# Performance work log

Hardware: AMD Instinct MI355X
Metric: run time of the kernel (lower is better)

## Reference

```python
import jax, jax.numpy as jnp
import numpy as np
import math

B, I, C = 64, 512, 32
PRED, PL, ST, NH = 96, 16, 8, 8
WKS = (24, 168, 336)
PN = (I + ST - PL) // ST + 1  # 64 patches (padding_patch='end')

def _gelu(x):
    return jax.nn.gelu(x, approximate=False)  # torch nn.GELU default (erf)

def _ln(x, g, b, eps=1e-5):
    m = x.mean(-1, keepdims=True)
    v = ((x - m) ** 2).mean(-1, keepdims=True)
    return (x - m) / jnp.sqrt(v + eps) * g + b

def setup_inputs() -> dict:
    keys = jax.random.split(jax.random.key(0), 64)
    ki = iter(keys)
    def nrm(sh, sc=0.02):
        return (jax.random.normal(next(ki), sh) * sc).astype(jnp.float32)
    inp = {}
    inp['s'] = jax.random.normal(next(ki), (B, I, C), jnp.float32)
    inp['t'] = jax.random.normal(next(ki), (B, I, C), jnp.float32)
    inp['cycle_index'] = jax.random.randint(next(ki), (B,), 0, 336)
    # router: Linear(C, C//2) -> GELU -> Linear(C//2, num_scales)
    inp['rw1'] = nrm((C // 2, C)); inp['rb1'] = jnp.zeros(C // 2)
    inp['rw2'] = nrm((3, C // 2)); inp['rb2'] = jnp.zeros(3)
    # per-scale amplitude / phase tables (Wk, C)
    inp['A0'] = nrm((WKS[0], C), 1.0); inp['A1'] = nrm((WKS[1], C), 1.0); inp['A2'] = nrm((WKS[2], C), 1.0)
    inp['P0'] = (jax.random.uniform(next(ki), (WKS[0], C)) * 2 * math.pi).astype(jnp.float32)
    inp['P1'] = (jax.random.uniform(next(ki), (WKS[1], C)) * 2 * math.pi).astype(jnp.float32)
    inp['P2'] = (jax.random.uniform(next(ki), (WKS[2], C)) * 2 * math.pi).astype(jnp.float32)
    # PB_RPA (phase-biased relative patch attention), n_embd=PL, n_head=NH
    inp['Wqkv'] = nrm((3 * PL, PL)); inp['bqkv'] = jnp.zeros(3 * PL)
    inp['Wo'] = nrm((PL, PL)); inp['bo'] = jnp.zeros(PL)
    inp['alpha'] = jnp.ones(())
    # bn2 over channel dim = patch_num
    inp['bn_g'] = jnp.ones(PN); inp['bn_b'] = jnp.zeros(PN)
    inp['W3'] = nrm((2 * PRED, PN * PL)); inp['b3'] = jnp.zeros(2 * PRED)
    inp['W4'] = nrm((PRED, 2 * PRED)); inp['b4'] = jnp.zeros(PRED)
    inp['W5'] = nrm((4 * PRED, I)); inp['b5'] = jnp.zeros(4 * PRED)
    inp['W6'] = nrm((PRED, 2 * PRED)); inp['b6'] = jnp.zeros(PRED)
    inp['W7'] = nrm((PRED, PRED // 2)); inp['b7'] = jnp.zeros(PRED)
    inp['W8'] = nrm((PRED, 2 * PRED)); inp['b8'] = jnp.zeros(PRED)
    inp['ln1_g'] = jnp.ones(2 * PRED); inp['ln1_b'] = jnp.zeros(2 * PRED)
    inp['ln2_g'] = jnp.ones(PRED // 2); inp['ln2_b'] = jnp.zeros(PRED // 2)
    # TrendEnhancer: Conv1d(C, C, 3, pad=1) gated residual
    inp['te_w'] = nrm((C, C, 3)); inp['te_b'] = jnp.zeros(C)
    return inp

def _forward(s, t, cycle_index, rw1, rb1, rw2, rb2, A0, A1, A2, P0, P1, P2,
             Wqkv, bqkv, Wo, bo, alpha, bn_g, bn_b, W3, b3, W4, b4, W5, b5,
             W6, b6, W7, b7, W8, b8, ln1_g, ln1_b, ln2_g, ln2_b, te_w, te_b):
    s = s.transpose(0, 2, 1)  # (B,C,I)
    t = t.transpose(0, 2, 1)
    # router -> per-scale softmax weights (B, num_scales)
    h = _gelu(s.mean(-1) @ rw1.T + rb1)
    p = jax.nn.softmax(h @ rw2.T + rb2, axis=-1)
    ar = jnp.arange(I)
    cs, ps = [], []
    for Atab, Ptab, Wk in ((A0, P0, WKS[0]), (A1, P1, WKS[1]), (A2, P2, WKS[2])):
        idx = (cycle_index[:, None] + ar) % Wk            # (B,I) data-dependent gather
        A = jax.nn.softplus(Atab[idx]).transpose(0, 2, 1)  # (B,C,I)
        phi = Ptab[idx].transpose(0, 2, 1)
        Qr = A * jnp.cos(phi)                              # Qi=A*sin(phi) is unused in hermitian_attn
        S = jnp.einsum('bcl,bck->blk', Qr, s) / math.sqrt(C)
        Aw = jax.nn.softmax(S, axis=-1)
        cs.append(jnp.einsum('blk,bck->bcl', Aw, s))
        ps.append(phi)
    c_stack = jnp.stack(cs, 1)    # (B,3,C,I)
    phi_stack = jnp.stack(ps, 1)
    beta = p[:, :, None, None]
    s = s + (beta * c_stack).sum(1)
    fused_phi = (beta * phi_stack).sum(1)  # (B,C,I)
    N = B * C
    s = s.reshape(N, I)
    t = t.reshape(N, I)
    phi = jnp.repeat(fused_phi.mean(1), C, axis=0)  # (N,I)
    # padding_patch='end' -> replicate-pad last `stride` steps
    s = jnp.concatenate([s, jnp.repeat(s[:, -1:], ST, 1)], 1)
    phi = jnp.concatenate([phi, jnp.repeat(phi[:, -1:], ST, 1)], 1)
    widx = jnp.arange(PN)[:, None] * ST + jnp.arange(PL)
    sp = s[:, widx]                # (N, PN, PL) unfold
    phis = phi[:, widx].mean(-1)   # (N, PN)
    # PB_RPA: MHA over patches with phase-difference bias
    qkv = sp @ Wqkv.T + bqkv
    q, k, v = jnp.split(qkv, 3, axis=-1)
    hd = PL // NH
    def heads(x):
        return x.reshape(N, PN, NH, hd).transpose(0, 2, 1, 3)
    q, k, v = heads(q), heads(k), heads(v)
    bias = alpha * jnp.cos(phis[:, None, :, None] - phis[:, None, None, :])  # (N,1,PN,PN)
    sc = jnp.einsum('nhtd,nhsd->nhts', q, k) / math.sqrt(hd) + bias
    Aw = jax.nn.softmax(sc, axis=-1)
    o = jnp.einsum('nhts,nhsd->nhtd', Aw, v).transpose(0, 2, 1, 3).reshape(N, PN, PL)
    o = o @ Wo.T + bo
    sx = _gelu(sp + o)
    # bn2: BatchNorm1d over channel=patch_num (training-mode batch stats)
    mu = sx.mean((0, 2), keepdims=True)
    var = ((sx - mu) ** 2).mean((0, 2), keepdims=True)
    sx = (sx - mu) / jnp.sqrt(var + 1e-5) * bn_g[None, :, None] + bn_b[None, :, None]
    sx = sx.reshape(N, PN * PL)
    sx = _gelu(sx @ W3.T + b3) @ W4.T + b4  # (N, PRED)
    # trend branch
    u = t @ W5.T + b5                       # (N, 4*PRED)
    u = u.reshape(N, 2 * PRED, 2).mean(-1)  # AvgPool1d(2)
    u = _ln(u, ln1_g, ln1_b)
    u = u @ W6.T + b6
    u = u.reshape(N, PRED // 2, 2).mean(-1)
    u = _ln(u, ln2_g, ln2_b)
    u = u @ W7.T + b7                       # (N, PRED)
    u = u.reshape(B, C, PRED)
    f = jnp.fft.rfft(u, axis=-1)
    mask = (jnp.arange(f.shape[-1]) < 5).astype(f.dtype)
    u = u + jnp.fft.irfft(f * mask, n=PRED, axis=-1)
    y = jax.lax.conv_general_dilated(u, te_w, (1,), [(1, 1)],
                                     dimension_numbers=('NCH', 'OIH', 'NCH')) + te_b[None, :, None]
    u = (u + _gelu(y)).reshape(N, PRED)     # TrendEnhancer gated-conv residual
    x = jnp.concatenate([sx, u], 1) @ W8.T + b8
    return x.reshape(B, C, PRED).transpose(0, 2, 1)  # (B, pred_len, C)

def reference(s, t, cycle_index, rw1, rb1, rw2, rb2, A0, A1, A2, P0, P1, P2,
              Wqkv, bqkv, Wo, bo, alpha, bn_g, bn_b, W3, b3, W4, b4, W5, b5,
              W6, b6, W7, b7, W8, b8, ln1_g, ln1_b, ln2_g, ln2_b, te_w, te_b):
    return _forward(s, t, cycle_index, rw1, rb1, rw2, rb2, A0, A1, A2, P0, P1, P2,
                    Wqkv, bqkv, Wo, bo, alpha, bn_g, bn_b, W3, b3, W4, b4, W5, b5,
                    W6, b6, W7, b7, W8, b8, ln1_g, ln1_b, ln2_g, ln2_b, te_w, te_b)
```

## Files before the change

### kernel.cpp

```cpp
#include <hip/hip_runtime.h>
#include <math.h>

#define B_    64
#define I_    512
#define C_    32
#define PRED_ 96
#define PL_   16
#define ST_   8
#define NH_   8
#define PN_   64
#define N_    2048

typedef short bf16x8 __attribute__((ext_vector_type(8)));
typedef float f32x4 __attribute__((ext_vector_type(4)));
typedef bf16x8 __attribute__((may_alias)) bf16x8_a;
typedef uint2 __attribute__((may_alias)) uint2_a;
typedef uint4 __attribute__((may_alias)) uint4_a;

__device__ __forceinline__ float geluf(float x) {
    return 0.5f * x * (1.0f + erff(x * 0.70710678118654752f));
}
__device__ __forceinline__ float softplusf(float x) {
    return fmaxf(x, 0.0f) + log1pf(__expf(-fabsf(x)));
}
__device__ __forceinline__ unsigned short f2bf(float x) {
    union { float f; unsigned int u; } v; v.f = x;
    unsigned int r = v.u + 0x7fffu + ((v.u >> 16) & 1u);
    return (unsigned short)(r >> 16);
}

__global__ void k_headphi(const float* __restrict__ s, const float* __restrict__ rw1,
                          const float* __restrict__ rb1, const float* __restrict__ rw2,
                          const float* __restrict__ rb2,
                          const float* __restrict__ P0, const float* __restrict__ P1,
                          const float* __restrict__ P2, const int* __restrict__ cyc,
                          float* __restrict__ wp, float* __restrict__ phis) {
    int b = blockIdx.x, t = threadIdx.x;
    __shared__ float part[8][32];
    __shared__ float smean[32];
    __shared__ float h[16];
    __shared__ float wpl[3];
    __shared__ float pm[I_];
    int c = t & 31, chunk = t >> 5;
    float acc = 0.f;
    for (int l = chunk * 64; l < chunk * 64 + 64; ++l)
        acc += s[((size_t)b * I_ + l) * C_ + c];
    part[chunk][c] = acc;
    __syncthreads();
    if (t < 32) {
        float v = 0.f;
#pragma unroll
        for (int i = 0; i < 8; ++i) v += part[i][t];
        smean[t] = v * (1.0f / I_);
    }
    __syncthreads();
    if (t < 16) {
        float a = rb1[t];
#pragma unroll
        for (int c2 = 0; c2 < 32; ++c2) a += smean[c2] * rw1[t * 32 + c2];
        h[t] = geluf(a);
    }
    __syncthreads();
    if (t == 0) {
        float lg[3], mx = -1e30f;
        for (int k = 0; k < 3; ++k) {
            float a = rb2[k];
            for (int j = 0; j < 16; ++j) a += h[j] * rw2[k * 16 + j];
            lg[k] = a; mx = fmaxf(mx, a);
        }
        float d = 0.f;
        for (int k = 0; k < 3; ++k) { lg[k] = __expf(lg[k] - mx); d += lg[k]; }
        float inv = 1.f / d;
        for (int k = 0; k < 3; ++k) { wpl[k] = lg[k] * inv; wp[b * 3 + k] = lg[k] * inv; }
    }
    __syncthreads();
    float p0 = wpl[0], p1 = wpl[1], p2 = wpl[2];
    int cy = cyc[b];
    for (int l = t; l < I_; l += 256) {
        float acc2 = 0.f;
        {
            int idx = (cy + l) % 24;
            const float4* r = (const float4*)(P0 + idx * 32);
            float s4 = 0.f;
#pragma unroll
            for (int i = 0; i < 8; ++i) { float4 v = r[i]; s4 += v.x + v.y + v.z + v.w; }
            acc2 += p0 * s4;
        }
        {
            int idx = (cy + l) % 168;
            const float4* r = (const float4*)(P1 + idx * 32);
            float s4 = 0.f;
#pragma unroll
            for (int i = 0; i < 8; ++i) { float4 v = r[i]; s4 += v.x + v.y + v.z + v.w; }
            acc2 += p1 * s4;
        }
        {
            int idx = (cy + l) % 336;
            const float4* r = (const float4*)(P2 + idx * 32);
            float s4 = 0.f;
#pragma unroll
            for (int i = 0; i < 8; ++i) { float4 v = r[i]; s4 += v.x + v.y + v.z + v.w; }
            acc2 += p2 * s4;
        }
        pm[l] = acc2 * (1.0f / 32.0f);
    }
    __syncthreads();
    if (t < PN_) {
        float sum = 0.f;
#pragma unroll
        for (int j = 0; j < 16; ++j) {
            int l = t * ST_ + j; if (l > 511) l = 511;
            sum += pm[l];
        }
        phis[b * PN_ + t] = sum * (1.0f / 16.0f);
    }
}

__global__ void __launch_bounds__(512) k_attn_mfma(
        const float* __restrict__ s, const int* __restrict__ cyc,
        const float* __restrict__ A0, const float* __restrict__ A1, const float* __restrict__ A2,
        const float* __restrict__ P0, const float* __restrict__ P1, const float* __restrict__ P2,
        float* __restrict__ pd, float* __restrict__ pcs) {
    int bx = blockIdx.x;
    int k3 = bx >> 1, kh = bx & 1;
    int b = blockIdx.y;
    int t = threadIdx.x;
    int wid = t >> 6, lane = t & 63;
    int l15 = lane & 15, lg = lane >> 4;

    __shared__ unsigned short s_lds[256][36];
    __shared__ unsigned short sT[32][262];
    __shared__ unsigned short Pt[8][16][36];

    {
        int row = t >> 1, half = t & 1;
        const float4* src = (const float4*)(s + ((size_t)b * I_ + kh * 256 + row) * C_ + half * 16);
        unsigned short bv[16];
#pragma unroll
        for (int i = 0; i < 4; ++i) {
            float4 v = src[i];
            bv[4 * i + 0] = f2bf(v.x); bv[4 * i + 1] = f2bf(v.y);
            bv[4 * i + 2] = f2bf(v.z); bv[4 * i + 3] = f2bf(v.w);
        }
#pragma unroll
        for (int i = 0; i < 2; ++i) {
            uint4 pk;
            pk.x = (unsigned)bv[8 * i + 0] | ((unsigned)bv[8 * i + 1] << 16);
            pk.y = (unsigned)bv[8 * i + 2] | ((unsigned)bv[8 * i + 3] << 16);
            pk.z = (unsigned)bv[8 * i + 4] | ((unsigned)bv[8 * i + 5] << 16);
            pk.w = (unsigned)bv[8 * i + 6] | ((unsigned)bv[8 * i + 7] << 16);
            *((uint4_a*)&s_lds[row][half * 16 + 8 * i]) = pk;
        }
#pragma unroll
        for (int cc = 0; cc < 16; ++cc) sT[half * 16 + cc][row] = bv[cc];
    }

    const float* Atab; const float* Ptab; int Wk;
    if (k3 == 0)      { Atab = A0; Ptab = P0; Wk = 24;  }
    else if (k3 == 1) { Atab = A1; Ptab = P1; Wk = 168; }
    else              { Atab = A2; Ptab = P2; Wk = 336; }
    int cy = cyc[b];
    bf16x8 qrf[4];
#pragma unroll
    for (int qt = 0; qt < 4; ++qt) {
        int q = wid * 64 + qt * 16 + l15;
        int idx = (cy + q) % Wk;
        const float4* Ar = (const float4*)(Atab + idx * 32 + lg * 8);
        const float4* Pr = (const float4*)(Ptab + idx * 32 + lg * 8);
        float4 a0 = Ar[0], a1 = Ar[1], p0 = Pr[0], p1 = Pr[1];
        float qv[8];
        qv[0] = softplusf(a0.x) * __cosf(p0.x);
        qv[1] = softplusf(a0.y) * __cosf(p0.y);
        qv[2] = softplusf(a0.z) * __cosf(p0.z);
        qv[3] = softplusf(a0.w) * __cosf(p0.w);
        qv[4] = softplusf(a1.x) * __cosf(p1.x);
        qv[5] = softplusf(a1.y) * __cosf(p1.y);
        qv[6] = softplusf(a1.z) * __cosf(p1.z);
        qv[7] = softplusf(a1.w) * __cosf(p1.w);
        bf16x8 f;
#pragma unroll
        for (int j = 0; j < 8; ++j) f[j] = (short)f2bf(qv[j]);
        qrf[qt] = f;
    }
    __syncthreads();

    const float rs = 0.17677669529663687f;
    f32x4 acc[4][2];
#pragma unroll
    for (int qt = 0; qt < 4; ++qt)
#pragma unroll
        for (int ct = 0; ct < 2; ++ct) acc[qt][ct] = (f32x4){0.f, 0.f, 0.f, 0.f};
    float dacc[4] = {0.f, 0.f, 0.f, 0.f};

    for (int kc = 0; kc < 8; ++kc) {
        int key0 = kc * 32;
        bf16x8 a0 = *((const bf16x8_a*)&s_lds[key0 + l15][lg * 8]);
        bf16x8 a1 = *((const bf16x8_a*)&s_lds[key0 + 16 + l15][lg * 8]);
        bf16x8 b0 = *((const bf16x8_a*)&sT[l15][key0 + lg * 8]);
        bf16x8 b1 = *((const bf16x8_a*)&sT[16 + l15][key0 + lg * 8]);
#pragma unroll
        for (int qt = 0; qt < 4; ++qt) {
            f32x4 st0 = __builtin_amdgcn_mfma_f32_16x16x32_bf16(a0, qrf[qt], (f32x4){0.f,0.f,0.f,0.f}, 0, 0, 0);
            f32x4 st1 = __builtin_amdgcn_mfma_f32_16x16x32_bf16(a1, qrf[qt], (f32x4){0.f,0.f,0.f,0.f}, 0, 0, 0);
#pragma unroll
            for (int h = 0; h < 2; ++h) {
                f32x4 sv = h ? st1 : st0;
                unsigned short pb[4];
                float ds = 0.f;
#pragma unroll
                for (int r = 0; r < 4; ++r) {
                    float e = __expf(sv[r] * rs);
                    unsigned short ub = f2bf(e);
                    pb[r] = ub;
                    union { unsigned int u; float f; } bb; bb.u = ((unsigned int)ub) << 16;
                    ds += bb.f;
                }
                dacc[qt] += ds;
                uint2 w2;
                w2.x = (unsigned)pb[0] | ((unsigned)pb[1] << 16);
                w2.y = (unsigned)pb[2] | ((unsigned)pb[3] << 16);
                *((uint2_a*)&Pt[wid][l15][h * 16 + lg * 4]) = w2;
            }
            bf16x8 pa = *((const bf16x8_a*)&Pt[wid][l15][lg * 8]);
            acc[qt][0] = __builtin_amdgcn_mfma_f32_16x16x32_bf16(pa, b0, acc[qt][0], 0, 0, 0);
            acc[qt][1] = __builtin_amdgcn_mfma_f32_16x16x32_bf16(pa, b1, acc[qt][1], 0, 0, 0);
        }
    }

    int hh = k3 * 2 + kh;
#pragma unroll
    for (int qt = 0; qt < 4; ++qt) {
        float dq = dacc[qt];
        dq += __shfl_xor(dq, 16);
        dq += __shfl_xor(dq, 32);
        int q = wid * 64 + qt * 16 + l15;
        if (lg == 0) pd[((size_t)hh * B_ + b) * I_ + q] = dq;
        int qbase = wid * 64 + qt * 16 + 4 * lg;
#pragma unroll
        for (int ct = 0; ct < 2; ++ct) {
            int c = ct * 16 + l15;
            float4 o;
            o.x = acc[qt][ct][0]; o.y = acc[qt][ct][1];
            o.z = acc[qt][ct][2]; o.w = acc[qt][ct][3];
            *(float4*)(pcs + (((size_t)hh * B_ + b) * C_ + c) * I_ + qbase) = o;
        }
    }
}

__global__ void k_combine(const float* __restrict__ s, const float* __restrict__ pd,
                          const float* __restrict__ pcs, const float* __restrict__ wp,
                          float* __restrict__ srow) {
    int b = blockIdx.x, l0 = blockIdx.y * 32;
    int tt_ = threadIdx.x;
    __shared__ float st[32][33];
    __shared__ float rw[3][32];
#pragma unroll
    for (int r = 0; r < 4; ++r) {
        int lin = r * 256 + tt_;
        int lq = lin >> 5, c = lin & 31;
        st[lq][c] = s[((size_t)b * I_ + l0 + lq) * C_ + c];
    }
    if (tt_ < 96) {
        int k3 = tt_ >> 5, lq = tt_ & 31;
        float d = pd[((size_t)(k3 * 2 + 0) * B_ + b) * I_ + l0 + lq]
                + pd[((size_t)(k3 * 2 + 1) * B_ + b) * I_ + l0 + lq];
        rw[k3][lq] = wp[b * 3 + k3] / d;
    }
    __syncthreads();
    const size_t CH = (size_t)B_ * C_ * I_;
#pragma unroll
    for (int r = 0; r < 4; ++r) {
        int lin = r * 256 + tt_;
        int co = lin >> 5, lo = lin & 31;
        size_t pi = ((size_t)b * C_ + co) * I_ + l0 + lo;
        float sum = 0.f;
#pragma unroll
        for (int k3 = 0; k3 < 3; ++k3) {
            float v = pcs[(2 * k3) * CH + pi] + pcs[(2 * k3 + 1) * CH + pi];
            sum += rw[k3][lo] * v;
        }
        srow[pi] = st[lo][co] + sum;
    }
}

__global__ void __launch_bounds__(256) k_patch(
        const float* __restrict__ srow, const float* __restrict__ phis,
        const float* __restrict__ Wqkv, const float* __restrict__ bqkv,
        const float* __restrict__ Wo, const float* __restrict__ bo,
        const float* __restrict__ alpha_p, float* __restrict__ sx) {
    int n = blockIdx.x, t = threadIdx.x;
    int p = t & 63, w = t >> 6;
    int lane = t & 63, l15 = lane & 15, lg = lane >> 4;
    int b = n >> 5;
    __shared__ float spl[64][17];
    __shared__ unsigned short spb[64][16];
    __shared__ unsigned short wqb[48][16];
    __shared__ unsigned short qkv2[36][72];
    __shared__ float vlf[16][68];
    __shared__ float o2l[64][18];
    __shared__ float wo[16][16];
    const float rs2 = 0.70710678118654752f;

    float alpha = alpha_p[0];
    const float* srn = srow + (size_t)n * I_;
#pragma unroll
    for (int jj = 0; jj < 4; ++jj) {
        int j = w * 4 + jj;
        int l = p * ST_ + j; if (l > 511) l = 511;
        float v = srn[l];
        spl[p][j] = v; spb[p][j] = f2bf(v);
    }
    for (int i = t; i < 768; i += 256) wqb[i >> 4][i & 15] = f2bf(Wqkv[i]);
    wo[t >> 4][t & 15] = Wo[t];
    if (t < 64) {
        float sv, cv;
        __sincosf(phis[b * PN_ + t], &sv, &cv);
        qkv2[32][t] = f2bf(cv); qkv2[33][t] = f2bf(sv);
        qkv2[34][t] = f2bf(alpha * cv); qkv2[35][t] = f2bf(alpha * sv);
    }
    __syncthreads();

    {
        bf16x8 af = {};
        if (lg < 2) af = *((const bf16x8_a*)&spb[w * 16 + l15][lg * 8]);
        f32x4 pacc[3];
#pragma unroll
        for (int nt = 0; nt < 3; ++nt) {
            bf16x8 wf = {};
            if (lg < 2) wf = *((const bf16x8_a*)&wqb[nt * 16 + l15][lg * 8]);
            pacc[nt] = __builtin_amdgcn_mfma_f32_16x16x32_bf16(af, wf, (f32x4){0.f,0.f,0.f,0.f}, 0, 0, 0);
        }
        __syncthreads();
#pragma unroll
        for (int nt = 0; nt < 3; ++nt) {
            int o = nt * 16 + l15;
            float bias = bqkv[o];
            float v0 = pacc[nt][0] + bias, v1 = pacc[nt][1] + bias;
            float v2 = pacc[nt][2] + bias, v3 = pacc[nt][3] + bias;
            int pb_ = w * 16 + 4 * lg;
            if (o < 16) {
                v0 *= rs2; v1 *= rs2; v2 *= rs2; v3 *= rs2;
                uint2 w2;
                w2.x = (unsigned)f2bf(v0) | ((unsigned)f2bf(v1) << 16);
                w2.y = (unsigned)f2bf(v2) | ((unsigned)f2bf(v3) << 16);
                *((uint2_a*)&qkv2[o][pb_]) = w2;
            } else if (o < 32) {
                uint2 w2;
                w2.x = (unsigned)f2bf(v0) | ((unsigned)f2bf(v1) << 16);
                w2.y = (unsigned)f2bf(v2) | ((unsigned)f2bf(v3) << 16);
                *((uint2_a*)&qkv2[o][pb_]) = w2;
            } else {
                *(float4*)&vlf[o - 32][pb_] = make_float4(v0, v1, v2, v3);
            }
        }
    }
    __syncthreads();

#pragma unroll
    for (int hh = 0; hh < 2; ++hh) {
        int h = 2 * w + hh;
        bf16x8 qf[4];
#pragma unroll
        for (int pt = 0; pt < 4; ++pt) {
            bf16x8 f = {};
            if (lg == 0) {
                int col = pt * 16 + l15;
                f[0] = (short)qkv2[2 * h][col];
                f[1] = (short)qkv2[2 * h + 1][col];
                f[2] = (short)qkv2[34][col];
                f[3] = (short)qkv2[35][col];
            }
            qf[pt] = f;
        }
        float o0a[4] = {0.f,0.f,0.f,0.f}, o1a[4] = {0.f,0.f,0.f,0.f}, da[4] = {0.f,0.f,0.f,0.f};
#pragma unroll
        for (int st = 0; st < 4; ++st) {
            bf16x8 kf = {};
            if (lg == 0) {
                int col = st * 16 + l15;
                kf[0] = (short)qkv2[16 + 2 * h][col];
                kf[1] = (short)qkv2[17 + 2 * h][col];
                kf[2] = (short)qkv2[32][col];
                kf[3] = (short)qkv2[33][col];
            }
            float4 v0 = *(const float4*)&vlf[2 * h][st * 16 + 4 * lg];
            float4 v1 = *(const float4*)&vlf[2 * h + 1][st * 16 + 4 * lg];
#pragma unroll
            for (int pt = 0; pt < 4; ++pt) {
                f32x4 sv = __builtin_amdgcn_mfma_f32_16x16x32_bf16(kf, qf[pt], (f32x4){0.f,0.f,0.f,0.f}, 0, 0, 0);
                float e0 = __expf(sv[0]), e1 = __expf(sv[1]);
                float e2 = __expf(sv[2]), e3 = __expf(sv[3]);
                da[pt] += e0 + e1 + e2 + e3;
                o0a[pt] += e0 * v0.x + e1 * v0.y + e2 * v0.z + e3 * v0.w;
                o1a[pt] += e0 * v1.x + e1 * v1.y + e2 * v1.z + e3 * v1.w;
            }
        }
#pragma unroll
        for (int pt = 0; pt < 4; ++pt) {
            float o0 = o0a[pt], o1 = o1a[pt], dd = da[pt];
            o0 += __shfl_xor(o0, 16); o0 += __shfl_xor(o0, 32);
            o1 += __shfl_xor(o1, 16); o1 += __shfl_xor(o1, 32);
            dd += __shfl_xor(dd, 16); dd += __shfl_xor(dd, 32);
            if (lg == 0) {
                float inv = 1.f / dd;
                *(float2*)&o2l[pt * 16 + l15][2 * h] = make_float2(o0 * inv, o1 * inv);
            }
        }
    }
    __syncthreads();

    float* sxr = sx + ((size_t)n * PN_ + p) * PL_;
#pragma unroll
    for (int ii = 0; ii < 4; ++ii) {
        int i2 = w * 4 + ii;
        float a = bo[i2];
#pragma unroll
        for (int j = 0; j < 16; ++j) a += o2l[p][j] * wo[i2][j];
        sxr[i2] = geluf(spl[p][i2] + a);
    }
}

__global__ void k_bn_stats(const float* __restrict__ sx, float* __restrict__ bnpart) {
    int pn = blockIdx.x, chunk = blockIdx.y, t = threadIdx.x;
    __shared__ float r1[256], r2[256];
    int j4 = t & 3, nb = t >> 2;
    float s1 = 0.f, s2 = 0.f;
    for (int i = 0; i < 8; ++i) {
        int n = chunk * 512 + nb + i * 64;
        float4 v = *(const float4*)(sx + ((size_t)n * PN_ + pn) * PL_ + j4 * 4);
        s1 += v.x + v.y + v.z + v.w;
        s2 += v.x * v.x + v.y * v.y + v.z * v.z + v.w * v.w;
    }
    r1[t] = s1; r2[t] = s2;
    __syncthreads();
    for (int st = 128; st > 0; st >>= 1) {
        if (t < st) { r1[t] += r1[t + st]; r2[t] += r2[t + st]; }
        __syncthreads();
    }
    if (t == 0) {
        bnpart[(pn * 4 + chunk) * 2 + 0] = r1[0];
        bnpart[(pn * 4 + chunk) * 2 + 1] = r2[0];
    }
}

template <int ACT, int FUSE_BN, int TRANS>
__global__ void __launch_bounds__(256) k_gemm_mfma(
        const float* __restrict__ A, const float* __restrict__ W,
        const float* __restrict__ bias, const float* __restrict__ bnpart,
        const float* __restrict__ bng, const float* __restrict__ bnb,
        float* __restrict__ Cout, int M, int Nn, int K) {
    __shared__ unsigned short Ab[64][36];
    __shared__ unsigned short Wb[64][36];
    __shared__ float bnm[64], bna[64];
    int bm = blockIdx.x * 64, bn = blockIdx.y * 64;
    int t = threadIdx.x;
    int wid = t >> 6, lane = t & 63, l15 = lane & 15, lg = lane >> 4;
    int srw = t >> 2, sk = (t & 3) * 8;
    if (FUSE_BN && t < 64) {
        float s1 = 0.f, s2 = 0.f;
#pragma unroll
        for (int ch = 0; ch < 4; ++ch) {
            s1 += bnpart[(t * 4 + ch) * 2 + 0];
            s2 += bnpart[(t * 4 + ch) * 2 + 1];
        }
        const float inv = 1.0f / (N_ * PL_);
        float mu = s1 * inv;
        float var = s2 * inv - mu * mu;
        float m = rsqrtf(var + 1e-5f) * bng[t];
        bnm[t] = m; bna[t] = bnb[t] - mu * m;
    }
    if (FUSE_BN) __syncthreads();
    f32x4 acc[4];
#pragma unroll
    for (int nt = 0; nt < 4; ++nt) acc[nt] = (f32x4){0.f, 0.f, 0.f, 0.f};

    for (int kt = 0; kt < K; kt += 32) {
        float4 av0, av1;
        if (TRANS) {
            int nrow = bm + srw;
            const float* tp = A + (size_t)(nrow >> 5) * (I_ * C_) + (nrow & 31);
            int l0 = kt + sk;
            av0.x = tp[(size_t)(l0 + 0) * C_]; av0.y = tp[(size_t)(l0 + 1) * C_];
            av0.z = tp[(size_t)(l0 + 2) * C_]; av0.w = tp[(size_t)(l0 + 3) * C_];
            av1.x = tp[(size_t)(l0 + 4) * C_]; av1.y = tp[(size_t)(l0 + 5) * C_];
            av1.z = tp[(size_t)(l0 + 6) * C_]; av1.w = tp[(size_t)(l0 + 7) * C_];
        } else {
            av0 = *(const float4*)(A + (size_t)(bm + srw) * K + kt + sk);
            av1 = *(const float4*)(A + (size_t)(bm + srw) * K + kt + sk + 4);
        }
        float4 wv0 = *(const float4*)(W + (size_t)(bn + srw) * K + kt + sk);
        float4 wv1 = *(const float4*)(W + (size_t)(bn + srw) * K + kt + sk + 4);
        if (FUSE_BN) {
            int pn = (kt + sk) >> 4;
            float m = bnm[pn], ad = bna[pn];
            av0.x = av0.x * m + ad; av0.y = av0.y * m + ad;
            av0.z = av0.z * m + ad; av0.w = av0.w * m + ad;
            av1.x = av1.x * m + ad; av1.y = av1.y * m + ad;
            av1.z = av1.z * m + ad; av1.w = av1.w * m + ad;
        }
        __syncthreads();
        {
            uint4 pk;
            pk.x = (unsigned)f2bf(av0.x) | ((unsigned)f2bf(av0.y) << 16);
            pk.y = (unsigned)f2bf(av0.z) | ((unsigned)f2bf(av0.w) << 16);
            pk.z = (unsigned)f2bf(av1.x) | ((unsigned)f2bf(av1.y) << 16);
            pk.w = (unsigned)f2bf(av1.z) | ((unsigned)f2bf(av1.w) << 16);
            *((uint4_a*)&Ab[srw][sk]) = pk;
            uint4 pw;
            pw.x = (unsigned)f2bf(wv0.x) | ((unsigned)f2bf(wv0.y) << 16);
            pw.y = (unsigned)f2bf(wv0.z) | ((unsigned)f2bf(wv0.w) << 16);
            pw.z = (unsigned)f2bf(wv1.x) | ((unsigned)f2bf(wv1.y) << 16);
            pw.w = (unsigned)f2bf(wv1.z) | ((unsigned)f2bf(wv1.w) << 16);
            *((uint4_a*)&Wb[srw][sk]) = pw;
        }
        __syncthreads();
        bf16x8 af = *((const bf16x8_a*)&Ab[wid * 16 + l15][lg * 8]);
#pragma unroll
        for (int nt = 0; nt < 4; ++nt) {
            bf16x8 wf = *((const bf16x8_a*)&Wb[nt * 16 + l15][lg * 8]);
            acc[nt] = __builtin_amdgcn_mfma_f32_16x16x32_bf16(af, wf, acc[nt], 0, 0, 0);
        }
    }
#pragma unroll
    for (int nt = 0; nt < 4; ++nt) {
#pragma unroll
        for (int r = 0; r < 4; ++r) {
            int m_ = bm + wid * 16 + 4 * lg + r;
            int n_ = bn + nt * 16 + l15;
            float v = acc[nt][r] + bias[n_];
            if (ACT) v = geluf(v);
            Cout[(size_t)m_ * Nn + n_] = v;
        }
    }
}

__global__ void k_rowmlp4(const float* __restrict__ g3, const float* __restrict__ W4,
                          const float* __restrict__ b4, float* __restrict__ sxf) {
    int n = blockIdx.x, t = threadIdx.x;
    __shared__ float row[192];
    for (int j = t; j < 192; j += 128) row[j] = g3[(size_t)n * 192 + j];
    __syncthreads();
    if (t < 96) {
        float a = b4[t];
        const float* wr = W4 + t * 192;
#pragma unroll 4
        for (int j = 0; j < 192; ++j) a += row[j] * wr[j];
        sxf[(size_t)n * 96 + t] = a;
    }
}

__global__ void k_u(const float* __restrict__ u1, const float* __restrict__ ln1g,
                    const float* __restrict__ ln1b, const float* __restrict__ W6,
                    const float* __restrict__ b6, const float* __restrict__ ln2g,
                    const float* __restrict__ ln2b, const float* __restrict__ W7,
                    const float* __restrict__ b7, float* __restrict__ u2out) {
    int n = blockIdx.x, t = threadIdx.x;
    __shared__ float a[192];
    __shared__ float red1[256], red2[256];
    __shared__ float c2[48];
    __shared__ float stat[2];
    __shared__ float u3l[96];
    __shared__ float cosb[5][96], sinb[5][96];
    __shared__ float coef[9];
    if (t < 96) {
#pragma unroll
        for (int k = 0; k < 5; ++k) {
            float sv, cv2;
            __sincosf(6.283185307179586f * (float)(k * t) / 96.0f, &sv, &cv2);
            cosb[k][t] = cv2; sinb[k][t] = sv;
        }
    }
    const float* ur = u1 + (size_t)n * 384;
    float av = 0.5f * (ur[2 * t] + ur[2 * t + 1]);
    red1[t] = av; red2[t] = av * av;
    if (t < 64) { red1[192 + t] = 0.f; red2[192 + t] = 0.f; }
    __syncthreads();
    for (int st = 128; st > 0; st >>= 1) {
        if (t < st) { red1[t] += red1[t + st]; red2[t] += red2[t + st]; }
        __syncthreads();
    }
    if (t == 0) {
        float mu = red1[0] * (1.0f / 192.0f);
        float var = red2[0] * (1.0f / 192.0f) - mu * mu;
        stat[0] = mu; stat[1] = rsqrtf(var + 1e-5f);
    }
    __syncthreads();
    a[t] = (av - stat[0]) * stat[1] * ln1g[t] + ln1b[t];
    __syncthreads();
    float bv = 0.f;
    if (t < 96) {
        bv = b6[t];
        const float* wr = W6 + t * 192;
#pragma unroll 4
        for (int j = 0; j < 192; ++j) bv += a[j] * wr[j];
    }
    __syncthreads();
    if (t < 96) red1[t] = bv;
    __syncthreads();
    float cv = 0.f;
    if (t < 48) cv = 0.5f * (red1[2 * t] + red1[2 * t + 1]);
    __syncthreads();
    if (t < 48) { red1[t] = cv; red2[t] = cv * cv; }
    else if (t < 64) { red1[t] = 0.f; red2[t] = 0.f; }
    __syncthreads();
    for (int st = 32; st > 0; st >>= 1) {
        if (t < st) { red1[t] += red1[t + st]; red2[t] += red2[t + st]; }
        __syncthreads();
    }
    if (t == 0) {
        float mu = red1[0] * (1.0f / 48.0f);
        float var = red2[0] * (1.0f / 48.0f) - mu * mu;
        stat[0] = mu; stat[1] = rsqrtf(var + 1e-5f);
    }
    __syncthreads();
    if (t < 48) c2[t] = (cv - stat[0]) * stat[1] * ln2g[t] + ln2b[t];
    __syncthreads();
    if (t < 96) {
        float acc = b7[t];
        const float* wr = W7 + t * 48;
#pragma unroll
        for (int j = 0; j < 48; ++j) acc += c2[j] * wr[j];
        u3l[t] = acc;
    }
    __syncthreads();
    if (t < 9) {
        int k = (t < 5) ? t : t - 4;
        const float* bas = (t < 5) ? cosb[k] : sinb[k];
        float acc = 0.f;
#pragma unroll 4
        for (int m = 0; m < 96; ++m) acc += u3l[m] * bas[m];
        coef[t] = acc;
    }
    __syncthreads();
    if (t < 96) {
        float rec = coef[0];
#pragma unroll
        for (int k = 1; k <= 4; ++k)
            rec += 2.0f * (coef[k] * cosb[k][t] + coef[4 + k] * sinb[k][t]);
        u2out[(size_t)n * 96 + t] = u3l[t] + rec * (1.0f / 96.0f);
    }
}

__global__ void k_conv(const float* __restrict__ u2, const float* __restrict__ tw,
                       const float* __restrict__ tb, float* __restrict__ u4) {
    int b = blockIdx.x, xq = blockIdx.y, t = threadIdx.x;
    int x0 = xq * 24;
    __shared__ float ub[32][26];
    __shared__ float twl[3072];
    for (int i = t; i < 832; i += 256) {
        int ic = i / 26, xx = i % 26;
        int gx = x0 + xx - 1;
        ub[ic][xx] = (gx >= 0 && gx < 96) ? u2[((size_t)b * 32 + ic) * 96 + gx] : 0.f;
    }
    for (int i = t; i < 3072; i += 256) twl[i] = tw[i];
    __syncthreads();
    for (int i = t; i < 768; i += 256) {
        int oc = i / 24, xx = i % 24;
        float acc = tb[oc];
#pragma unroll 8
        for (int ic = 0; ic < 32; ++ic) {
            const float* wv = twl + (oc * 32 + ic) * 3;
            acc += ub[ic][xx] * wv[0] + ub[ic][xx + 1] * wv[1] + ub[ic][xx + 2] * wv[2];
        }
        u4[((size_t)b * 32 + oc) * 96 + x0 + xx] = ub[oc][xx + 1] + geluf(acc);
    }
}

__global__ void k_out(const float* __restrict__ sxf, const float* __restrict__ u4,
                      const float* __restrict__ W8, const float* __restrict__ b8,
                      float* __restrict__ out) {
    int b = blockIdx.x, oq = blockIdx.y, t = threadIdx.x;
    __shared__ float ld[32][193];
    for (int i = t; i < 32 * 96; i += 256) {
        int c = i / 96, j = i % 96;
        ld[c][j]      = sxf[((size_t)(b * 32 + c)) * 96 + j];
        ld[c][96 + j] = u4[((size_t)(b * 32 + c)) * 96 + j];
    }
    __syncthreads();
    for (int i = t; i < 24 * 32; i += 256) {
        int o = oq * 24 + (i >> 5), c = i & 31;
        float acc = b8[o];
        const float* wr = W8 + o * 192;
#pragma unroll 4
        for (int j = 0; j < 192; ++j) acc += ld[c][j] * wr[j];
        out[((size_t)b * 96 + o) * 32 + c] = acc;
    }
}

extern "C" void kernel_launch(void* const* d_in, const int* in_sizes, int n_in,
                              void* d_out, int out_size, void* d_ws, size_t ws_size,
                              hipStream_t stream) {
    const float* s    = (const float*)d_in[0];
    const float* t    = (const float*)d_in[1];
    const int*   cyc  = (const int*)d_in[2];
    const float* rw1  = (const float*)d_in[3];
    const float* rb1  = (const float*)d_in[4];
    const float* rw2  = (const float*)d_in[5];
    const float* rb2  = (const float*)d_in[6];
    const float* A0   = (const float*)d_in[7];
    const float* A1   = (const float*)d_in[8];
    const float* A2   = (const float*)d_in[9];
    const float* P0   = (const float*)d_in[10];
    const float* P1   = (const float*)d_in[11];
    const float* P2   = (const float*)d_in[12];
    const float* Wqkv = (const float*)d_in[13];
    const float* bqkv = (const float*)d_in[14];
    const float* Wo   = (const float*)d_in[15];
    const float* bo   = (const float*)d_in[16];
    const float* alpha= (const float*)d_in[17];
    const float* bn_g = (const float*)d_in[18];
    const float* bn_b = (const float*)d_in[19];
    const float* W3   = (const float*)d_in[20];
    const float* b3   = (const float*)d_in[21];
    const float* W4   = (const float*)d_in[22];
    const float* b4   = (const float*)d_in[23];
    const float* W5   = (const float*)d_in[24];
    const float* b5   = (const float*)d_in[25];
    const float* W6   = (const float*)d_in[26];
    const float* b6   = (const float*)d_in[27];
    const float* W7   = (const float*)d_in[28];
    const float* b7   = (const float*)d_in[29];
    const float* W8   = (const float*)d_in[30];
    const float* b8   = (const float*)d_in[31];
    const float* ln1g = (const float*)d_in[32];
    const float* ln1b = (const float*)d_in[33];
    const float* ln2g = (const float*)d_in[34];
    const float* ln2b = (const float*)d_in[35];
    const float* tew  = (const float*)d_in[36];
    const float* teb  = (const float*)d_in[37];

    float* ws     = (float*)d_ws;
    float* wp     = ws;
    float* phis   = ws + 192;
    float* bnpart = ws + 4288;
    float* srow   = ws + 4800;
    float* R      = srow + 1048576;
    float* pd  = R;
    float* pcs = R + 196608;
    float* sx  = R;
    float* g3  = R + 2097152;
    float* sxf = R + 2490368;
    float* u1  = R + 2686976;
    float* u2f = R + 3473408;
    float* u4f = R + 3670016;
    float* out = (float*)d_out;

    k_headphi<<<64, 256, 0, stream>>>(s, rw1, rb1, rw2, rb2, P0, P1, P2, cyc, wp, phis);
    k_attn_mfma<<<dim3(6, 64), 512, 0, stream>>>(s, cyc, A0, A1, A2, P0, P1, P2, pd, pcs);
    k_combine<<<dim3(64, 16), 256, 0, stream>>>(s, pd, pcs, wp, srow);
    k_patch<<<2048, 256, 0, stream>>>(srow, phis, Wqkv, bqkv, Wo, bo, alpha, sx);
    k_bn_stats<<<dim3(64, 4), 256, 0, stream>>>(sx, bnpart);
    k_gemm_mfma<1, 1, 0><<<dim3(32, 3), 256, 0, stream>>>(sx, W3, b3, bnpart, bn_g, bn_b, g3, 2048, 192, 1024);
    k_rowmlp4<<<2048, 128, 0, stream>>>(g3, W4, b4, sxf);
    k_gemm_mfma<0, 0, 1><<<dim3(32, 6), 256, 0, stream>>>(t, W5, b5, bnpart, bn_g, bn_b, u1, 2048, 384, 512);
    k_u<<<2048, 192, 0, stream>>>(u1, ln1g, ln1b, W6, b6, ln2g, ln2b, W7, b7, u2f);
    k_conv<<<dim3(64, 4), 256, 0, stream>>>(u2f, tew, teb, u4f);
    k_out<<<dim3(64, 4), 256, 0, stream>>>(sxf, u4f, W8, b8, out);
}
```

Before: 355.7 us.

## Split attention queries across blocks, pre-transpose t, use packed bf16 conversion

The attention kernel now launches 256-thread blocks with a new grid dimension that splits the 512 queries into two halves. Each block still loads and converts all 256 keys, so key staging is duplicated in exchange for twice as many blocks. The softmax scale is folded into the query vectors, and the denominator now sums the fp32 exponentials instead of bf16-rounded ones, which slightly changes numerics. Separately, k_combine writes a transposed copy of t so the W5 GEMM reads rows contiguously instead of strided gathers, and float-to-bf16 conversion uses the packed HIP intrinsics.

```diff
diff --git a/kernel.cpp b/kernel.cpp
--- a/kernel.cpp
+++ b/kernel.cpp
@@ -1,4 +1,5 @@
 #include <hip/hip_runtime.h>
+#include <hip/hip_bf16.h>
 #include <math.h>
 
 #define B_    64
@@ -24,9 +25,14 @@
     return fmaxf(x, 0.0f) + log1pf(__expf(-fabsf(x)));
 }
 __device__ __forceinline__ unsigned short f2bf(float x) {
-    union { float f; unsigned int u; } v; v.f = x;
-    unsigned int r = v.u + 0x7fffu + ((v.u >> 16) & 1u);
-    return (unsigned short)(r >> 16);
+    union { __hip_bfloat16 h; unsigned short u; } v;
+    v.h = __float2bfloat16(x);
+    return v.u;
+}
+__device__ __forceinline__ unsigned pk2bf(float lo, float hi) {
+    union { __hip_bfloat162 h; unsigned u; } v;
+    v.h = __float22bfloat162_rn(make_float2(lo, hi));
+    return v.u;
 }
 
 __global__ void k_headphi(const float* __restrict__ s, const float* __restrict__ rw1,
@@ -116,43 +122,44 @@
     }
 }
 
-__global__ void __launch_bounds__(512) k_attn_mfma(
+__global__ void __launch_bounds__(256) k_attn_mfma(
         const float* __restrict__ s, const int* __restrict__ cyc,
         const float* __restrict__ A0, const float* __restrict__ A1, const float* __restrict__ A2,
         const float* __restrict__ P0, const float* __restrict__ P1, const float* __restrict__ P2,
         float* __restrict__ pd, float* __restrict__ pcs) {
     int bx = blockIdx.x;
     int k3 = bx >> 1, kh = bx & 1;
-    int b = blockIdx.y;
+    int qh = blockIdx.y;
+    int b = blockIdx.z;
     int t = threadIdx.x;
     int wid = t >> 6, lane = t & 63;
     int l15 = lane & 15, lg = lane >> 4;
 
     __shared__ unsigned short s_lds[256][36];
     __shared__ unsigned short sT[32][262];
-    __shared__ unsigned short Pt[8][16][36];
+    __shared__ unsigned short Pt[4][16][36];
 
     {
-        int row = t >> 1, half = t & 1;
-        const float4* src = (const float4*)(s + ((size_t)b * I_ + kh * 256 + row) * C_ + half * 16);
-        unsigned short bv[16];
-#pragma unroll
-        for (int i = 0; i < 4; ++i) {
+        int row = t;
+        const float4* src = (const float4*)(s + ((size_t)b * I_ + kh * 256 + row) * C_);
+        unsigned short bv[32];
+#pragma unroll
+        for (int i = 0; i < 8; ++i) {
             float4 v = src[i];
             bv[4 * i + 0] = f2bf(v.x); bv[4 * i + 1] = f2bf(v.y);
             bv[4 * i + 2] = f2bf(v.z); bv[4 * i + 3] = f2bf(v.w);
         }
 #pragma unroll
-        for (int i = 0; i < 2; ++i) {
+        for (int i = 0; i < 4; ++i) {
             uint4 pk;
             pk.x = (unsigned)bv[8 * i + 0] | ((unsigned)bv[8 * i + 1] << 16);
             pk.y = (unsigned)bv[8 * i + 2] | ((unsigned)bv[8 * i + 3] << 16);
             pk.z = (unsigned)bv[8 * i + 4] | ((unsigned)bv[8 * i + 5] << 16);
             pk.w = (unsigned)bv[8 * i + 6] | ((unsigned)bv[8 * i + 7] << 16);
-            *((uint4_a*)&s_lds[row][half * 16 + 8 * i]) = pk;
-        }
-#pragma unroll
-        for (int cc = 0; cc < 16; ++cc) sT[half * 16 + cc][row] = bv[cc];
+            *((uint4_a*)&s_lds[row][8 * i]) = pk;
+        }
+#pragma unroll
+        for (int cc = 0; cc < 32; ++cc) sT[cc][row] = bv[cc];
     }
 
     const float* Atab; const float* Ptab; int Wk;
@@ -160,23 +167,24 @@
     else if (k3 == 1) { Atab = A1; Ptab = P1; Wk = 168; }
     else              { Atab = A2; Ptab = P2; Wk = 336; }
     int cy = cyc[b];
+    const float rs = 0.17677669529663687f;
     bf16x8 qrf[4];
 #pragma unroll
     for (int qt = 0; qt < 4; ++qt) {
-        int q = wid * 64 + qt * 16 + l15;
+        int q = qh * 256 + wid * 64 + qt * 16 + l15;
         int idx = (cy + q) % Wk;
         const float4* Ar = (const float4*)(Atab + idx * 32 + lg * 8);
         const float4* Pr = (const float4*)(Ptab + idx * 32 + lg * 8);
         float4 a0 = Ar[0], a1 = Ar[1], p0 = Pr[0], p1 = Pr[1];
         float qv[8];
-        qv[0] = softplusf(a0.x) * __cosf(p0.x);
-        qv[1] = softplusf(a0.y) * __cosf(p0.y);
-        qv[2] = softplusf(a0.z) * __cosf(p0.z);
-        qv[3] = softplusf(a0.w) * __cosf(p0.w);
-        qv[4] = softplusf(a1.x) * __cosf(p1.x);
-        qv[5] = softplusf(a1.y) * __cosf(p1.y);
-        qv[6] = softplusf(a1.z) * __cosf(p1.z);
-        qv[7] = softplusf(a1.w) * __cosf(p1.w);
+        qv[0] = rs * softplusf(a0.x) * __cosf(p0.x);
+        qv[1] = rs * softplusf(a0.y) * __cosf(p0.y);
+        qv[2] = rs * softplusf(a0.z) * __cosf(p0.z);
+        qv[3] = rs * softplusf(a0.w) * __cosf(p0.w);
+        qv[4] = rs * softplusf(a1.x) * __cosf(p1.x);
+        qv[5] = rs * softplusf(a1.y) * __cosf(p1.y);
+        qv[6] = rs * softplusf(a1.z) * __cosf(p1.z);
+        qv[7] = rs * softplusf(a1.w) * __cosf(p1.w);
         bf16x8 f;
 #pragma unroll
         for (int j = 0; j < 8; ++j) f[j] = (short)f2bf(qv[j]);
@@ -184,7 +192,6 @@
     }
     __syncthreads();
 
-    const float rs = 0.17677669529663687f;
     f32x4 acc[4][2];
 #pragma unroll
     for (int qt = 0; qt < 4; ++qt)
@@ -202,24 +209,21 @@
         for (int qt = 0; qt < 4; ++qt) {
             f32x4 st0 = __builtin_amdgcn_mfma_f32_16x16x32_bf16(a0, qrf[qt], (f32x4){0.f,0.f,0.f,0.f}, 0, 0, 0);
             f32x4 st1 = __builtin_amdgcn_mfma_f32_16x16x32_bf16(a1, qrf[qt], (f32x4){0.f,0.f,0.f,0.f}, 0, 0, 0);
-#pragma unroll
-            for (int h = 0; h < 2; ++h) {
-                f32x4 sv = h ? st1 : st0;
-                unsigned short pb[4];
-                float ds = 0.f;
-#pragma unroll
-                for (int r = 0; r < 4; ++r) {
-                    float e = __expf(sv[r] * rs);
-                    unsigned short ub = f2bf(e);
-                    pb[r] = ub;
-                    union { unsigned int u; float f; } bb; bb.u = ((unsigned int)ub) << 16;
-                    ds += bb.f;
-                }
-                dacc[qt] += ds;
+            {
+                float e0 = __expf(st0[0]), e1 = __expf(st0[1]);
+                float e2 = __expf(st0[2]), e3 = __expf(st0[3]);
+                dacc[qt] += (e0 + e1) + (e2 + e3);
                 uint2 w2;
-                w2.x = (unsigned)pb[0] | ((unsigned)pb[1] << 16);
-                w2.y = (unsigned)pb[2] | ((unsigned)pb[3] << 16);
-                *((uint2_a*)&Pt[wid][l15][h * 16 + lg * 4]) = w2;
+                w2.x = pk2bf(e0, e1); w2.y = pk2bf(e2, e3);
+                *((uint2_a*)&Pt[wid][l15][lg * 4]) = w2;
+            }
+            {
+                float e0 = __expf(st1[0]), e1 = __expf(st1[1]);
+                float e2 = __expf(st1[2]), e3 = __expf(st1[3]);
+                dacc[qt] += (e0 + e1) + (e2 + e3);
+                uint2 w2;
+                w2.x = pk2bf(e0, e1); w2.y = pk2bf(e2, e3);
+                *((uint2_a*)&Pt[wid][l15][16 + lg * 4]) = w2;
             }
             bf16x8 pa = *((const bf16x8_a*)&Pt[wid][l15][lg * 8]);
             acc[qt][0] = __builtin_amdgcn_mfma_f32_16x16x32_bf16(pa, b0, acc[qt][0], 0, 0, 0);
@@ -233,9 +237,9 @@
         float dq = dacc[qt];
         dq += __shfl_xor(dq, 16);
         dq += __shfl_xor(dq, 32);
-        int q = wid * 64 + qt * 16 + l15;
+        int q = qh * 256 + wid * 64 + qt * 16 + l15;
         if (lg == 0) pd[((size_t)hh * B_ + b) * I_ + q] = dq;
-        int qbase = wid * 64 + qt * 16 + 4 * lg;
+        int qbase = qh * 256 + wid * 64 + qt * 16 + 4 * lg;
 #pragma unroll
         for (int ct = 0; ct < 2; ++ct) {
             int c = ct * 16 + l15;
@@ -247,18 +251,20 @@
     }
 }
 
-__global__ void k_combine(const float* __restrict__ s, const float* __restrict__ pd,
-                          const float* __restrict__ pcs, const float* __restrict__ wp,
-                          float* __restrict__ srow) {
+__global__ void k_combine(const float* __restrict__ s, const float* __restrict__ t,
+                          const float* __restrict__ pd, const float* __restrict__ pcs,
+                          const float* __restrict__ wp,
+                          float* __restrict__ srow, float* __restrict__ trow) {
     int b = blockIdx.x, l0 = blockIdx.y * 32;
     int tt_ = threadIdx.x;
-    __shared__ float st[32][33];
+    __shared__ float st[32][33], tl[32][33];
     __shared__ float rw[3][32];
 #pragma unroll
     for (int r = 0; r < 4; ++r) {
         int lin = r * 256 + tt_;
         int lq = lin >> 5, c = lin & 31;
         st[lq][c] = s[((size_t)b * I_ + l0 + lq) * C_ + c];
+        tl[lq][c] = t[((size_t)b * I_ + l0 + lq) * C_ + c];
     }
     if (tt_ < 96) {
         int k3 = tt_ >> 5, lq = tt_ & 31;
@@ -280,6 +286,7 @@
             sum += rw[k3][lo] * v;
         }
         srow[pi] = st[lo][co] + sum;
+        trow[pi] = tl[lo][co];
     }
 }
 
@@ -443,7 +450,7 @@
     }
 }
 
-template <int ACT, int FUSE_BN, int TRANS>
+template <int ACT, int FUSE_BN>
 __global__ void __launch_bounds__(256) k_gemm_mfma(
         const float* __restrict__ A, const float* __restrict__ W,
         const float* __restrict__ bias, const float* __restrict__ bnpart,
@@ -475,19 +482,8 @@
     for (int nt = 0; nt < 4; ++nt) acc[nt] = (f32x4){0.f, 0.f, 0.f, 0.f};
 
     for (int kt = 0; kt < K; kt += 32) {
-        float4 av0, av1;
-        if (TRANS) {
-            int nrow = bm + srw;
-            const float* tp = A + (size_t)(nrow >> 5) * (I_ * C_) + (nrow & 31);
-            int l0 = kt + sk;
-            av0.x = tp[(size_t)(l0 + 0) * C_]; av0.y = tp[(size_t)(l0 + 1) * C_];
-            av0.z = tp[(size_t)(l0 + 2) * C_]; av0.w = tp[(size_t)(l0 + 3) * C_];
-            av1.x = tp[(size_t)(l0 + 4) * C_]; av1.y = tp[(size_t)(l0 + 5) * C_];
-            av1.z = tp[(size_t)(l0 + 6) * C_]; av1.w = tp[(size_t)(l0 + 7) * C_];
-        } else {
-            av0 = *(const float4*)(A + (size_t)(bm + srw) * K + kt + sk);
-            av1 = *(const float4*)(A + (size_t)(bm + srw) * K + kt + sk + 4);
-        }
+        float4 av0 = *(const float4*)(A + (size_t)(bm + srw) * K + kt + sk);
+        float4 av1 = *(const float4*)(A + (size_t)(bm + srw) * K + kt + sk + 4);
         float4 wv0 = *(const float4*)(W + (size_t)(bn + srw) * K + kt + sk);
         float4 wv1 = *(const float4*)(W + (size_t)(bn + srw) * K + kt + sk + 4);
         if (FUSE_BN) {
@@ -501,16 +497,16 @@
         __syncthreads();
         {
             uint4 pk;
-            pk.x = (unsigned)f2bf(av0.x) | ((unsigned)f2bf(av0.y) << 16);
-            pk.y = (unsigned)f2bf(av0.z) | ((unsigned)f2bf(av0.w) << 16);
-            pk.z = (unsigned)f2bf(av1.x) | ((unsigned)f2bf(av1.y) << 16);
-            pk.w = (unsigned)f2bf(av1.z) | ((unsigned)f2bf(av1.w) << 16);
+            pk.x = pk2bf(av0.x, av0.y);
+            pk.y = pk2bf(av0.z, av0.w);
+            pk.z = pk2bf(av1.x, av1.y);
+            pk.w = pk2bf(av1.z, av1.w);
             *((uint4_a*)&Ab[srw][sk]) = pk;
             uint4 pw;
-            pw.x = (unsigned)f2bf(wv0.x) | ((unsigned)f2bf(wv0.y) << 16);
-            pw.y = (unsigned)f2bf(wv0.z) | ((unsigned)f2bf(wv0.w) << 16);
-            pw.z = (unsigned)f2bf(wv1.x) | ((unsigned)f2bf(wv1.y) << 16);
-            pw.w = (unsigned)f2bf(wv1.z) | ((unsigned)f2bf(wv1.w) << 16);
+            pw.x = pk2bf(wv0.x, wv0.y);
+            pw.y = pk2bf(wv0.z, wv0.w);
+            pw.z = pk2bf(wv1.x, wv1.y);
+            pw.w = pk2bf(wv1.z, wv1.w);
             *((uint4_a*)&Wb[srw][sk]) = pw;
         }
         __syncthreads();
@@ -734,7 +730,8 @@
     float* phis   = ws + 192;
     float* bnpart = ws + 4288;
     float* srow   = ws + 4800;
-    float* R      = srow + 1048576;
+    float* trow   = srow + 1048576;
+    float* R      = trow + 1048576;
     float* pd  = R;
     float* pcs = R + 196608;
     float* sx  = R;
@@ -746,13 +743,13 @@
     float* out = (float*)d_out;
 
     k_headphi<<<64, 256, 0, stream>>>(s, rw1, rb1, rw2, rb2, P0, P1, P2, cyc, wp, phis);
-    k_attn_mfma<<<dim3(6, 64), 512, 0, stream>>>(s, cyc, A0, A1, A2, P0, P1, P2, pd, pcs);
-    k_combine<<<dim3(64, 16), 256, 0, stream>>>(s, pd, pcs, wp, srow);
+    k_attn_mfma<<<dim3(6, 2, 64), 256, 0, stream>>>(s, cyc, A0, A1, A2, P0, P1, P2, pd, pcs);
+    k_combine<<<dim3(64, 16), 256, 0, stream>>>(s, t, pd, pcs, wp, srow, trow);
     k_patch<<<2048, 256, 0, stream>>>(srow, phis, Wqkv, bqkv, Wo, bo, alpha, sx);
     k_bn_stats<<<dim3(64, 4), 256, 0, stream>>>(sx, bnpart);
-    k_gemm_mfma<1, 1, 0><<<dim3(32, 3), 256, 0, stream>>>(sx, W3, b3, bnpart, bn_g, bn_b, g3, 2048, 192, 1024);
+    k_gemm_mfma<1, 1><<<dim3(32, 3), 256, 0, stream>>>(sx, W3, b3, bnpart, bn_g, bn_b, g3, 2048, 192, 1024);
     k_rowmlp4<<<2048, 128, 0, stream>>>(g3, W4, b4, sxf);
-    k_gemm_mfma<0, 0, 1><<<dim3(32, 6), 256, 0, stream>>>(t, W5, b5, bnpart, bn_g, bn_b, u1, 2048, 384, 512);
+    k_gemm_mfma<0, 0><<<dim3(32, 6), 256, 0, stream>>>(trow, W5, b5, bnpart, bn_g, bn_b, u1, 2048, 384, 512);
     k_u<<<2048, 192, 0, stream>>>(u1, ln1g, ln1b, W6, b6, ln2g, ln2b, W7, b7, u2f);
     k_conv<<<dim3(64, 4), 256, 0, stream>>>(u2f, tew, teb, u4f);
     k_out<<<dim3(64, 4), 256, 0, stream>>>(sxf, u4f, W8, b8, out);
```

After: 350.3 us. No clear change (-1.5%).
